# Optimization experiments

Measured on AMD Instinct MI355X. Metric: run time of the kernel, lower is better.

## Reference

```python
import jax, jax.numpy as jnp
import numpy as np

B = 65536
IN1, H, KOUT, GRID, OUT = 784, 128, 64, 10, 10
RICKER_C = 2.0 / (np.sqrt(3.0) * np.pi ** 0.25)


def setup_inputs() -> dict:
    key = jax.random.key(0)
    ks = jax.random.split(key, 8)
    x = jax.random.normal(ks[0], (B, IN1), dtype=jnp.float32)
    w1 = jax.random.normal(ks[1], (H, IN1), dtype=jnp.float32) / np.sqrt(IN1)
    b1 = jnp.zeros((H,), dtype=jnp.float32)
    # wavelet-KAN coefficients: (out, in, gridsize)
    coef = jax.random.normal(ks[2], (KOUT, H, GRID), dtype=jnp.float32) / (
        np.sqrt(H) * np.sqrt(GRID))
    wbias = jnp.zeros((KOUT,), dtype=jnp.float32)
    w2 = jax.random.normal(ks[3], (OUT, KOUT), dtype=jnp.float32) / np.sqrt(KOUT)
    b2 = jnp.zeros((OUT,), dtype=jnp.float32)
    return {"x": x, "w1": w1, "b1": b1, "coef": coef, "wbias": wbias,
            "w2": w2, "b2": b2}


def _ricker(t):
    # Mexican-hat mother wavelet
    return RICKER_C * (1.0 - t * t) * jnp.exp(-0.5 * t * t)


def reference(x, w1, b1, coef, wbias, w2, b2):
    h = x @ w1.T + b1                               # (B, H)
    k = jnp.arange(1, GRID + 1, dtype=h.dtype)      # scales 1..grid
    psi = _ricker(h[:, :, None] * k)                # (B, H, GRID)
    y = jnp.einsum('big,oig->bo', psi, coef) + wbias  # (B, KOUT)
    return y @ w2.T + b2                            # (B, OUT)
```

## Files before the change

kernel.cpp:

```cpp
#include <hip/hip_runtime.h>

#define STRH 132

typedef short bf16x8 __attribute__((ext_vector_type(8)));
typedef float f32x4 __attribute__((ext_vector_type(4)));

#define MFMA16(a, b, c) __builtin_amdgcn_mfma_f32_16x16x32_bf16((a), (b), (c), 0, 0, 0)

__device__ __forceinline__ unsigned int f2bf_rne(float f) {
    unsigned int u = __float_as_uint(f);
    return (u + 0x7FFFu + ((u >> 16) & 1u)) >> 16;
}
__device__ __forceinline__ float bfbits2f(unsigned int b) {
    return __uint_as_float(b << 16);
}
__device__ __forceinline__ unsigned int pack_hu(float a, float b) {
    unsigned int ua = (__float_as_uint(a) + 0x8000u) >> 16;
    unsigned int ub = (__float_as_uint(b) + 0x8000u) >> 16;
    return ua | (ub << 16);
}
__device__ __forceinline__ uint4 pack8(const unsigned int* b) {
    return make_uint4(b[0] | (b[1] << 16), b[2] | (b[3] << 16),
                      b[4] | (b[5] << 16), b[6] | (b[7] << 16));
}

#define WS_BYTES_NEEDED 451072

__global__ __launch_bounds__(256) void prep_kernel(
    const float* __restrict__ coef, const float* __restrict__ wbias,
    const float* __restrict__ w2, const float* __restrict__ b2,
    const float* __restrict__ w1, float* __restrict__ ws, int do_w1)
{
    int idx = blockIdx.x * 256 + threadIdx.x;
    if (idx < 20480) {
        int l = (idx >> 3) & 63, j = idx & 7;
        int s = idx >> 9;
        int n = l & 15, q = l >> 4;
        int P = 4 * s + q;
        int g = P >> 4;
        int i = ((P & 15) << 3) + j;
        float v = 0.f;
        if (n < 10) {
            float sum = 0.f;
            const float* cp = coef + i * 10 + g;
            const float* wp = w2 + n * 64;
            #pragma unroll 8
            for (int o = 0; o < 64; ++o)
                sum = fmaf(wp[o], cp[o * 1280], sum);
            v = 0.8673250706f * sum;
        }
        ((unsigned short*)ws)[idx] = (unsigned short)f2bf_rne(v);
    } else if (idx < 20490) {
        int n = idx - 20480;
        float sum = b2[n];
        for (int o = 0; o < 64; ++o)
            sum = fmaf(w2[n * 64 + o], wbias[o], sum);
        ws[10240 + n] = sum;
    } else if (do_w1 && idx >= 20736) {
        int t = idx - 20736;
        if (t < 102400) {
            int n = t / 800, k = t - n * 800;
            unsigned int hi = 0, lo = 0;
            if (k < 784) {
                float f = w1[n * 784 + k];
                hi = f2bf_rne(f);
                lo = f2bf_rne(f - bfbits2f(hi));
            }
            ((unsigned short*)((char*)ws + 41472))[t] = (unsigned short)hi;
            ((unsigned short*)((char*)ws + 246272))[t] = (unsigned short)lo;
        }
    }
}

union StageU {
    struct {
        unsigned short xa_hi[2048], xa_lo[2048];
        unsigned short wb_hi[4096], wb_lo[4096];
    } p1;
    unsigned short c2[10240];
};

template <bool WSW1>
__global__ __launch_bounds__(256) void mnist_fused(
    const float* __restrict__ x, const float* __restrict__ w1,
    const float* __restrict__ b1, const float* __restrict__ ws,
    float* __restrict__ out)
{
    __shared__ float h_tile[64 * STRH];
    __shared__ StageU u;

    const int tid  = threadIdx.x;
    const int lane = tid & 63;
    const int wv   = tid >> 6;
    const long row0 = (long)blockIdx.x * 64;

    const int sr = tid >> 2, so = tid & 3;
    const int wn = tid >> 1, whh = tid & 1;

    const float* xbase = x + (row0 + sr) * 784 + so * 8;
    const unsigned short* w1hi = (const unsigned short*)((const char*)ws + 41472);
    const unsigned short* w1lo = (const unsigned short*)((const char*)ws + 246272);

    f32x4 acc[8];
    #pragma unroll
    for (int T = 0; T < 8; ++T)
        acc[T] = (f32x4){0.f, 0.f, 0.f, 0.f};

    float4 xr0 = ((const float4*)xbase)[0];
    float4 xr1 = ((const float4*)xbase)[1];
    uint4 wh0, wh1, wl0, wl1;
    float4 wf0, wf1, wf2, wf3;
    if (WSW1) {
        const unsigned short* ph = w1hi + wn * 800 + whh * 16;
        const unsigned short* pl = w1lo + wn * 800 + whh * 16;
        wh0 = *(const uint4*)ph;       wh1 = *(const uint4*)(ph + 8);
        wl0 = *(const uint4*)pl;       wl1 = *(const uint4*)(pl + 8);
    } else {
        const float* pw = w1 + wn * 784 + whh * 16;
        wf0 = ((const float4*)pw)[0]; wf1 = ((const float4*)pw)[1];
        wf2 = ((const float4*)pw)[2]; wf3 = ((const float4*)pw)[3];
    }

    for (int kt = 0; kt < 25; ++kt) {
        __syncthreads();
        {
            float xf[8] = {xr0.x, xr0.y, xr0.z, xr0.w, xr1.x, xr1.y, xr1.z, xr1.w};
            unsigned int hb[8], lb[8];
            #pragma unroll
            for (int e = 0; e < 8; ++e) {
                hb[e] = f2bf_rne(xf[e]);
                lb[e] = f2bf_rne(xf[e] - bfbits2f(hb[e]));
            }
            int xi = ((sr >> 4) * 64 + so * 16 + (sr & 15)) * 8;
            *(uint4*)&u.p1.xa_hi[xi] = pack8(hb);
            *(uint4*)&u.p1.xa_lo[xi] = pack8(lb);
        }
        {
            int wi0 = ((wn >> 4) * 64 + (2 * whh) * 16 + (wn & 15)) * 8;
            if (WSW1) {
                *(uint4*)&u.p1.wb_hi[wi0]       = wh0;
                *(uint4*)&u.p1.wb_hi[wi0 + 128] = wh1;
                *(uint4*)&u.p1.wb_lo[wi0]       = wl0;
                *(uint4*)&u.p1.wb_lo[wi0 + 128] = wl1;
            } else {
                float wf[16] = {wf0.x, wf0.y, wf0.z, wf0.w, wf1.x, wf1.y, wf1.z, wf1.w,
                                wf2.x, wf2.y, wf2.z, wf2.w, wf3.x, wf3.y, wf3.z, wf3.w};
                unsigned int hb[16], lb[16];
                #pragma unroll
                for (int e = 0; e < 16; ++e) {
                    hb[e] = f2bf_rne(wf[e]);
                    lb[e] = f2bf_rne(wf[e] - bfbits2f(hb[e]));
                }
                *(uint4*)&u.p1.wb_hi[wi0]       = pack8(hb);
                *(uint4*)&u.p1.wb_hi[wi0 + 128] = pack8(hb + 8);
                *(uint4*)&u.p1.wb_lo[wi0]       = pack8(lb);
                *(uint4*)&u.p1.wb_lo[wi0 + 128] = pack8(lb + 8);
            }
        }
        __syncthreads();
        if (kt < 24) {
            int kn = (kt + 1) * 32;
            bool xv = (kn + so * 8) < 784;
            const float4* xp = (const float4*)(xv ? (xbase + kn) : x);
            xr0 = xp[0]; xr1 = xp[1];
            if (!xv) { xr0 = make_float4(0.f, 0.f, 0.f, 0.f); xr1 = xr0; }
            if (WSW1) {
                const unsigned short* ph = w1hi + wn * 800 + kn + whh * 16;
                const unsigned short* pl = w1lo + wn * 800 + kn + whh * 16;
                wh0 = *(const uint4*)ph;  wh1 = *(const uint4*)(ph + 8);
                wl0 = *(const uint4*)pl;  wl1 = *(const uint4*)(pl + 8);
            } else {
                int kw = kn + whh * 16;
                bool wvld = kw < 784;
                const float* pw = wvld ? (w1 + wn * 784 + kw) : w1;
                wf0 = ((const float4*)pw)[0]; wf1 = ((const float4*)pw)[1];
                wf2 = ((const float4*)pw)[2]; wf3 = ((const float4*)pw)[3];
                if (!wvld) {
                    wf0 = make_float4(0.f, 0.f, 0.f, 0.f);
                    wf1 = wf0; wf2 = wf0; wf3 = wf0;
                }
            }
        }
        {
            uint4 ta = *(const uint4*)&u.p1.xa_hi[(wv * 64 + lane) * 8];
            uint4 tb = *(const uint4*)&u.p1.xa_lo[(wv * 64 + lane) * 8];
            bf16x8 Ah = __builtin_bit_cast(bf16x8, ta);
            bf16x8 Al = __builtin_bit_cast(bf16x8, tb);
            #pragma unroll
            for (int T = 0; T < 8; ++T) {
                uint4 th = *(const uint4*)&u.p1.wb_hi[(T * 64 + lane) * 8];
                uint4 tl = *(const uint4*)&u.p1.wb_lo[(T * 64 + lane) * 8];
                bf16x8 Bh = __builtin_bit_cast(bf16x8, th);
                bf16x8 Bl = __builtin_bit_cast(bf16x8, tl);
                acc[T] = MFMA16(Ah, Bh, acc[T]);
                acc[T] = MFMA16(Ah, Bl, acc[T]);
                acc[T] = MFMA16(Al, Bh, acc[T]);
            }
        }
    }

    {
        const int mb = wv * 16 + (lane >> 4) * 4;
        const int nb = lane & 15;
        #pragma unroll
        for (int T = 0; T < 8; ++T) {
            float bias = b1[T * 16 + nb];
            #pragma unroll
            for (int r = 0; r < 4; ++r)
                h_tile[(mb + r) * STRH + T * 16 + nb] = acc[T][r] + bias;
        }
    }

    f32x4 acc2 = (f32x4){0.f, 0.f, 0.f, 0.f};
    const int q = lane >> 4;
    const float* hrow = h_tile + (wv * 16 + (lane & 15)) * STRH;

    for (int half = 0; half < 2; ++half) {
        __syncthreads();
        {
            const uint4* src = (const uint4*)ws + half * 1280 + tid;
            uint4* dst = (uint4*)u.c2 + tid;
            #pragma unroll
            for (int c = 0; c < 5; ++c) dst[c * 256] = src[c * 256];
        }
        __syncthreads();
        #pragma unroll 4
        for (int s2 = 0; s2 < 20; ++s2) {
            int P = (half * 20 + s2) * 4 + q;
            float kg = (float)((P >> 4) + 1);
            int i0 = (P & 15) << 3;
            float4 h0 = *(const float4*)(hrow + i0);
            float4 h1 = *(const float4*)(hrow + i0 + 4);
            float hv[8] = {h0.x, h0.y, h0.z, h0.w, h1.x, h1.y, h1.z, h1.w};
            unsigned int pk[4];
            #pragma unroll
            for (int e = 0; e < 8; e += 2) {
                float t0 = hv[e] * kg,   t1 = hv[e + 1] * kg;
                float q0 = t0 * t0,      q1 = t1 * t1;
                float p0 = (1.f - q0) * __expf(-0.5f * q0);
                float p1 = (1.f - q1) * __expf(-0.5f * q1);
                pk[e >> 1] = pack_hu(p0, p1);
            }
            bf16x8 A = __builtin_bit_cast(bf16x8, make_uint4(pk[0], pk[1], pk[2], pk[3]));
            uint4 braw = *(const uint4*)&u.c2[(s2 * 64 + lane) * 8];
            bf16x8 Bf = __builtin_bit_cast(bf16x8, braw);
            acc2 = MFMA16(A, Bf, acc2);
        }
    }

    {
        const int n = lane & 15;
        if (n < 10) {
            float bias2 = ws[10240 + n];
            const long rb = row0 + wv * 16 + (lane >> 4) * 4;
            #pragma unroll
            for (int r = 0; r < 4; ++r)
                out[(rb + r) * 10 + n] = acc2[r] + bias2;
        }
    }
}

extern "C" void kernel_launch(void* const* d_in, const int* in_sizes, int n_in,
                              void* d_out, int out_size, void* d_ws, size_t ws_size,
                              hipStream_t stream) {
    const float* x     = (const float*)d_in[0];
    const float* w1    = (const float*)d_in[1];
    const float* b1    = (const float*)d_in[2];
    const float* coef  = (const float*)d_in[3];
    const float* wbias = (const float*)d_in[4];
    const float* w2    = (const float*)d_in[5];
    const float* b2    = (const float*)d_in[6];
    float* out = (float*)d_out;
    float* ws  = (float*)d_ws;

    const int Brows = in_sizes[0] / 784;
    const bool wsw1 = ws_size >= (size_t)WS_BYTES_NEEDED;

    prep_kernel<<<wsw1 ? 481 : 81, 256, 0, stream>>>(coef, wbias, w2, b2, w1, ws,
                                                     wsw1 ? 1 : 0);
    if (wsw1)
        mnist_fused<true><<<Brows / 64, 256, 0, stream>>>(x, w1, b1, ws, out);
    else
        mnist_fused<false><<<Brows / 64, 256, 0, stream>>>(x, w1, b1, ws, out);
}
```

Before: 349.7 us.

## Replace split-bf16 first GEMM with single fp16 MFMA reading x directly

The first GEMM moves from a three-pass hi/lo bf16 split to a single fp16 MFMA pass. Activations are loaded straight from global memory into registers, and w1 is read from a pre-swizzled fp16 workspace layout. This drops the LDS staging and both per-k-tile barriers, and stores h in LDS as fp16 with a wider stride. The first coefficient tile is also prefetched before the GEMM, and occupancy is raised via launch bounds. The trade-off is lower precision in the first layer and in h, plus the loss of the fallback path for small workspaces.

```diff
diff --git a/kernel.cpp b/kernel.cpp
--- a/kernel.cpp
+++ b/kernel.cpp
@@ -1,35 +1,31 @@
 #include <hip/hip_runtime.h>
 
-#define STRH 132
-
 typedef short bf16x8 __attribute__((ext_vector_type(8)));
+typedef _Float16 f16x8 __attribute__((ext_vector_type(8)));
 typedef float f32x4 __attribute__((ext_vector_type(4)));
 
-#define MFMA16(a, b, c) __builtin_amdgcn_mfma_f32_16x16x32_bf16((a), (b), (c), 0, 0, 0)
+#define MFMA_BF16(a, b, c) __builtin_amdgcn_mfma_f32_16x16x32_bf16((a), (b), (c), 0, 0, 0)
+#define MFMA_F16(a, b, c)  __builtin_amdgcn_mfma_f32_16x16x32_f16((a), (b), (c), 0, 0, 0)
+
+#define STRH 136
 
 __device__ __forceinline__ unsigned int f2bf_rne(float f) {
     unsigned int u = __float_as_uint(f);
     return (u + 0x7FFFu + ((u >> 16) & 1u)) >> 16;
-}
-__device__ __forceinline__ float bfbits2f(unsigned int b) {
-    return __uint_as_float(b << 16);
 }
 __device__ __forceinline__ unsigned int pack_hu(float a, float b) {
     unsigned int ua = (__float_as_uint(a) + 0x8000u) >> 16;
     unsigned int ub = (__float_as_uint(b) + 0x8000u) >> 16;
     return ua | (ub << 16);
 }
-__device__ __forceinline__ uint4 pack8(const unsigned int* b) {
-    return make_uint4(b[0] | (b[1] << 16), b[2] | (b[3] << 16),
-                      b[4] | (b[5] << 16), b[6] | (b[7] << 16));
-}
-
-#define WS_BYTES_NEEDED 451072
+__device__ __forceinline__ unsigned int pkrtz(float a, float b) {
+    return __builtin_bit_cast(unsigned int, __builtin_amdgcn_cvt_pkrtz(a, b));
+}
 
 __global__ __launch_bounds__(256) void prep_kernel(
     const float* __restrict__ coef, const float* __restrict__ wbias,
     const float* __restrict__ w2, const float* __restrict__ b2,
-    const float* __restrict__ w1, float* __restrict__ ws, int do_w1)
+    const float* __restrict__ w1, float* __restrict__ ws)
 {
     int idx = blockIdx.x * 256 + threadIdx.x;
     if (idx < 20480) {
@@ -56,207 +52,136 @@
         for (int o = 0; o < 64; ++o)
             sum = fmaf(w2[n * 64 + o], wbias[o], sum);
         ws[10240 + n] = sum;
-    } else if (do_w1 && idx >= 20736) {
+    } else if (idx >= 20736) {
         int t = idx - 20736;
         if (t < 102400) {
             int n = t / 800, k = t - n * 800;
-            unsigned int hi = 0, lo = 0;
-            if (k < 784) {
-                float f = w1[n * 784 + k];
-                hi = f2bf_rne(f);
-                lo = f2bf_rne(f - bfbits2f(hi));
-            }
-            ((unsigned short*)((char*)ws + 41472))[t] = (unsigned short)hi;
-            ((unsigned short*)((char*)ws + 246272))[t] = (unsigned short)lo;
-        }
-    }
-}
-
-union StageU {
-    struct {
-        unsigned short xa_hi[2048], xa_lo[2048];
-        unsigned short wb_hi[4096], wb_lo[4096];
-    } p1;
-    unsigned short c2[10240];
-};
-
-template <bool WSW1>
-__global__ __launch_bounds__(256) void mnist_fused(
-    const float* __restrict__ x, const float* __restrict__ w1,
-    const float* __restrict__ b1, const float* __restrict__ ws,
-    float* __restrict__ out)
+            _Float16 hv = (_Float16)0.f;
+            if (k < 784) hv = (_Float16)w1[n * 784 + k];
+            int kt = k >> 5, ko = k & 31;
+            int qq = ko >> 3, j = ko & 7;
+            int T = n >> 4, ln = qq * 16 + (n & 15);
+            int slot = ((kt * 8 + T) * 64 + ln) * 8 + j;
+            ((unsigned short*)((char*)ws + 41472))[slot] =
+                __builtin_bit_cast(unsigned short, hv);
+        }
+    }
+}
+
+__global__ __launch_bounds__(256, 4) void mnist_fused(
+    const float* __restrict__ x, const float* __restrict__ b1,
+    const float* __restrict__ ws, float* __restrict__ out)
 {
-    __shared__ float h_tile[64 * STRH];
-    __shared__ StageU u;
+    __shared__ __align__(16) unsigned short h_tile[64 * STRH];
+    __shared__ __align__(16) unsigned short c2buf[10240];
 
     const int tid  = threadIdx.x;
     const int lane = tid & 63;
     const int wv   = tid >> 6;
+    const int m    = lane & 15;
+    const int q    = lane >> 4;
     const long row0 = (long)blockIdx.x * 64;
 
-    const int sr = tid >> 2, so = tid & 3;
-    const int wn = tid >> 1, whh = tid & 1;
-
-    const float* xbase = x + (row0 + sr) * 784 + so * 8;
-    const unsigned short* w1hi = (const unsigned short*)((const char*)ws + 41472);
-    const unsigned short* w1lo = (const unsigned short*)((const char*)ws + 246272);
+    {
+        const uint4* src = (const uint4*)ws + tid;
+        uint4* dst = (uint4*)c2buf + tid;
+        #pragma unroll
+        for (int c = 0; c < 5; ++c) dst[c * 256] = src[c * 256];
+    }
+
+    const unsigned short* w1f = (const unsigned short*)((const char*)ws + 41472);
+    const float* pa = x + (row0 + wv * 16 + m) * 784 + q * 8;
 
     f32x4 acc[8];
     #pragma unroll
-    for (int T = 0; T < 8; ++T)
-        acc[T] = (f32x4){0.f, 0.f, 0.f, 0.f};
-
-    float4 xr0 = ((const float4*)xbase)[0];
-    float4 xr1 = ((const float4*)xbase)[1];
-    uint4 wh0, wh1, wl0, wl1;
-    float4 wf0, wf1, wf2, wf3;
-    if (WSW1) {
-        const unsigned short* ph = w1hi + wn * 800 + whh * 16;
-        const unsigned short* pl = w1lo + wn * 800 + whh * 16;
-        wh0 = *(const uint4*)ph;       wh1 = *(const uint4*)(ph + 8);
-        wl0 = *(const uint4*)pl;       wl1 = *(const uint4*)(pl + 8);
-    } else {
-        const float* pw = w1 + wn * 784 + whh * 16;
-        wf0 = ((const float4*)pw)[0]; wf1 = ((const float4*)pw)[1];
-        wf2 = ((const float4*)pw)[2]; wf3 = ((const float4*)pw)[3];
-    }
-
-    for (int kt = 0; kt < 25; ++kt) {
-        __syncthreads();
-        {
-            float xf[8] = {xr0.x, xr0.y, xr0.z, xr0.w, xr1.x, xr1.y, xr1.z, xr1.w};
-            unsigned int hb[8], lb[8];
+    for (int T = 0; T < 8; ++T) acc[T] = (f32x4){0.f, 0.f, 0.f, 0.f};
+
+    for (int kt = 0; kt < 24; ++kt) {
+        float4 a0 = *(const float4*)(pa + kt * 32);
+        float4 a1 = *(const float4*)(pa + kt * 32 + 4);
+        uint4 b[8];
+        #pragma unroll
+        for (int T = 0; T < 8; ++T)
+            b[T] = *(const uint4*)(w1f + kt * 4096 + T * 512 + lane * 8);
+        uint4 ap = make_uint4(pkrtz(a0.x, a0.y), pkrtz(a0.z, a0.w),
+                              pkrtz(a1.x, a1.y), pkrtz(a1.z, a1.w));
+        f16x8 A = __builtin_bit_cast(f16x8, ap);
+        #pragma unroll
+        for (int T = 0; T < 8; ++T)
+            acc[T] = MFMA_F16(A, __builtin_bit_cast(f16x8, b[T]), acc[T]);
+    }
+    {
+        float4 z4 = make_float4(0.f, 0.f, 0.f, 0.f);
+        const float* ps = (q < 2) ? (pa + 768) : pa;
+        float4 a0 = (q < 2) ? *(const float4*)(ps)     : z4;
+        float4 a1 = (q < 2) ? *(const float4*)(ps + 4) : z4;
+        uint4 b[8];
+        #pragma unroll
+        for (int T = 0; T < 8; ++T)
+            b[T] = *(const uint4*)(w1f + 24 * 4096 + T * 512 + lane * 8);
+        uint4 ap = make_uint4(pkrtz(a0.x, a0.y), pkrtz(a0.z, a0.w),
+                              pkrtz(a1.x, a1.y), pkrtz(a1.z, a1.w));
+        f16x8 A = __builtin_bit_cast(f16x8, ap);
+        #pragma unroll
+        for (int T = 0; T < 8; ++T)
+            acc[T] = MFMA_F16(A, __builtin_bit_cast(f16x8, b[T]), acc[T]);
+    }
+
+    {
+        #pragma unroll
+        for (int T = 0; T < 8; ++T) {
+            float bias = b1[T * 16 + m];
             #pragma unroll
-            for (int e = 0; e < 8; ++e) {
-                hb[e] = f2bf_rne(xf[e]);
-                lb[e] = f2bf_rne(xf[e] - bfbits2f(hb[e]));
+            for (int r = 0; r < 4; ++r) {
+                _Float16 hv = (_Float16)(acc[T][r] + bias);
+                h_tile[(wv * 16 + q * 4 + r) * STRH + T * 16 + m] =
+                    __builtin_bit_cast(unsigned short, hv);
             }
-            int xi = ((sr >> 4) * 64 + so * 16 + (sr & 15)) * 8;
-            *(uint4*)&u.p1.xa_hi[xi] = pack8(hb);
-            *(uint4*)&u.p1.xa_lo[xi] = pack8(lb);
-        }
-        {
-            int wi0 = ((wn >> 4) * 64 + (2 * whh) * 16 + (wn & 15)) * 8;
-            if (WSW1) {
-                *(uint4*)&u.p1.wb_hi[wi0]       = wh0;
-                *(uint4*)&u.p1.wb_hi[wi0 + 128] = wh1;
-                *(uint4*)&u.p1.wb_lo[wi0]       = wl0;
-                *(uint4*)&u.p1.wb_lo[wi0 + 128] = wl1;
-            } else {
-                float wf[16] = {wf0.x, wf0.y, wf0.z, wf0.w, wf1.x, wf1.y, wf1.z, wf1.w,
-                                wf2.x, wf2.y, wf2.z, wf2.w, wf3.x, wf3.y, wf3.z, wf3.w};
-                unsigned int hb[16], lb[16];
-                #pragma unroll
-                for (int e = 0; e < 16; ++e) {
-                    hb[e] = f2bf_rne(wf[e]);
-                    lb[e] = f2bf_rne(wf[e] - bfbits2f(hb[e]));
-                }
-                *(uint4*)&u.p1.wb_hi[wi0]       = pack8(hb);
-                *(uint4*)&u.p1.wb_hi[wi0 + 128] = pack8(hb + 8);
-                *(uint4*)&u.p1.wb_lo[wi0]       = pack8(lb);
-                *(uint4*)&u.p1.wb_lo[wi0 + 128] = pack8(lb + 8);
-            }
-        }
-        __syncthreads();
-        if (kt < 24) {
-            int kn = (kt + 1) * 32;
-            bool xv = (kn + so * 8) < 784;
-            const float4* xp = (const float4*)(xv ? (xbase + kn) : x);
-            xr0 = xp[0]; xr1 = xp[1];
-            if (!xv) { xr0 = make_float4(0.f, 0.f, 0.f, 0.f); xr1 = xr0; }
-            if (WSW1) {
-                const unsigned short* ph = w1hi + wn * 800 + kn + whh * 16;
-                const unsigned short* pl = w1lo + wn * 800 + kn + whh * 16;
-                wh0 = *(const uint4*)ph;  wh1 = *(const uint4*)(ph + 8);
-                wl0 = *(const uint4*)pl;  wl1 = *(const uint4*)(pl + 8);
-            } else {
-                int kw = kn + whh * 16;
-                bool wvld = kw < 784;
-                const float* pw = wvld ? (w1 + wn * 784 + kw) : w1;
-                wf0 = ((const float4*)pw)[0]; wf1 = ((const float4*)pw)[1];
-                wf2 = ((const float4*)pw)[2]; wf3 = ((const float4*)pw)[3];
-                if (!wvld) {
-                    wf0 = make_float4(0.f, 0.f, 0.f, 0.f);
-                    wf1 = wf0; wf2 = wf0; wf3 = wf0;
-                }
-            }
-        }
-        {
-            uint4 ta = *(const uint4*)&u.p1.xa_hi[(wv * 64 + lane) * 8];
-            uint4 tb = *(const uint4*)&u.p1.xa_lo[(wv * 64 + lane) * 8];
-            bf16x8 Ah = __builtin_bit_cast(bf16x8, ta);
-            bf16x8 Al = __builtin_bit_cast(bf16x8, tb);
-            #pragma unroll
-            for (int T = 0; T < 8; ++T) {
-                uint4 th = *(const uint4*)&u.p1.wb_hi[(T * 64 + lane) * 8];
-                uint4 tl = *(const uint4*)&u.p1.wb_lo[(T * 64 + lane) * 8];
-                bf16x8 Bh = __builtin_bit_cast(bf16x8, th);
-                bf16x8 Bl = __builtin_bit_cast(bf16x8, tl);
-                acc[T] = MFMA16(Ah, Bh, acc[T]);
-                acc[T] = MFMA16(Ah, Bl, acc[T]);
-                acc[T] = MFMA16(Al, Bh, acc[T]);
-            }
-        }
-    }
-
-    {
-        const int mb = wv * 16 + (lane >> 4) * 4;
-        const int nb = lane & 15;
-        #pragma unroll
-        for (int T = 0; T < 8; ++T) {
-            float bias = b1[T * 16 + nb];
-            #pragma unroll
-            for (int r = 0; r < 4; ++r)
-                h_tile[(mb + r) * STRH + T * 16 + nb] = acc[T][r] + bias;
         }
     }
 
     f32x4 acc2 = (f32x4){0.f, 0.f, 0.f, 0.f};
-    const int q = lane >> 4;
-    const float* hrow = h_tile + (wv * 16 + (lane & 15)) * STRH;
-
-    for (int half = 0; half < 2; ++half) {
-        __syncthreads();
-        {
-            const uint4* src = (const uint4*)ws + half * 1280 + tid;
-            uint4* dst = (uint4*)u.c2 + tid;
+    const unsigned short* hrow = h_tile + (wv * 16 + m) * STRH;
+
+    #pragma unroll
+    for (int half_ = 0; half_ < 2; ++half_) {
+        if (half_ == 1) {
+            __syncthreads();
+            const uint4* src = (const uint4*)ws + 1280 + tid;
+            uint4* dst = (uint4*)c2buf + tid;
             #pragma unroll
             for (int c = 0; c < 5; ++c) dst[c * 256] = src[c * 256];
         }
         __syncthreads();
         #pragma unroll 4
         for (int s2 = 0; s2 < 20; ++s2) {
-            int P = (half * 20 + s2) * 4 + q;
+            int P = (half_ * 20 + s2) * 4 + q;
             float kg = (float)((P >> 4) + 1);
             int i0 = (P & 15) << 3;
-            float4 h0 = *(const float4*)(hrow + i0);
-            float4 h1 = *(const float4*)(hrow + i0 + 4);
-            float hv[8] = {h0.x, h0.y, h0.z, h0.w, h1.x, h1.y, h1.z, h1.w};
+            uint4 hraw = *(const uint4*)(hrow + i0);
+            f16x8 hh = __builtin_bit_cast(f16x8, hraw);
             unsigned int pk[4];
             #pragma unroll
             for (int e = 0; e < 8; e += 2) {
-                float t0 = hv[e] * kg,   t1 = hv[e + 1] * kg;
-                float q0 = t0 * t0,      q1 = t1 * t1;
-                float p0 = (1.f - q0) * __expf(-0.5f * q0);
-                float p1 = (1.f - q1) * __expf(-0.5f * q1);
+                float t0 = (float)hh[e] * kg;
+                float t1 = (float)hh[e + 1] * kg;
+                float z0 = t0 * t0, z1 = t1 * t1;
+                float p0 = (1.f - z0) * __expf(-0.5f * z0);
+                float p1 = (1.f - z1) * __expf(-0.5f * z1);
                 pk[e >> 1] = pack_hu(p0, p1);
             }
             bf16x8 A = __builtin_bit_cast(bf16x8, make_uint4(pk[0], pk[1], pk[2], pk[3]));
-            uint4 braw = *(const uint4*)&u.c2[(s2 * 64 + lane) * 8];
-            bf16x8 Bf = __builtin_bit_cast(bf16x8, braw);
-            acc2 = MFMA16(A, Bf, acc2);
-        }
-    }
-
-    {
-        const int n = lane & 15;
-        if (n < 10) {
-            float bias2 = ws[10240 + n];
-            const long rb = row0 + wv * 16 + (lane >> 4) * 4;
-            #pragma unroll
-            for (int r = 0; r < 4; ++r)
-                out[(rb + r) * 10 + n] = acc2[r] + bias2;
-        }
+            uint4 braw = *(const uint4*)&c2buf[(s2 * 64 + lane) * 8];
+            acc2 = MFMA_BF16(A, __builtin_bit_cast(bf16x8, braw), acc2);
+        }
+    }
+
+    if (m < 10) {
+        float bias2 = ws[10240 + m];
+        const long rb = row0 + wv * 16 + q * 4;
+        #pragma unroll
+        for (int r = 0; r < 4; ++r)
+            out[(rb + r) * 10 + m] = acc2[r] + bias2;
     }
 }
 
@@ -274,12 +199,6 @@
     float* ws  = (float*)d_ws;
 
     const int Brows = in_sizes[0] / 784;
-    const bool wsw1 = ws_size >= (size_t)WS_BYTES_NEEDED;
-
-    prep_kernel<<<wsw1 ? 481 : 81, 256, 0, stream>>>(coef, wbias, w2, b2, w1, ws,
-                                                     wsw1 ? 1 : 0);
-    if (wsw1)
-        mnist_fused<true><<<Brows / 64, 256, 0, stream>>>(x, w1, b1, ws, out);
-    else
-        mnist_fused<false><<<Brows / 64, 256, 0, stream>>>(x, w1, b1, ws, out);
-}
+    prep_kernel<<<481, 256, 0, stream>>>(coef, wbias, w2, b2, w1, ws);
+    mnist_fused<<<Brows / 64, 256, 0, stream>>>(x, b1, ws, out);
+}
```

Result: no change. 345.4 us (-1.2%).
